# Optimization experiments

Measured on AMD Instinct MI355X. Metric: run time of the kernel, lower is better.

## Reference

```python
import jax, jax.numpy as jnp
import numpy as np

RMAX = 5.0   # max_radius
NB = 8       # bessel bases
NSH = 9      # (lmax+1)^2, lmax=2
S = 4        # message passing steps


def _rms(x):
    return x * jax.lax.rsqrt(jnp.mean(x * x, axis=-1, keepdims=True) + 1e-6)


def _mlp(x, w1, b1, w2, b2):
    # 2-layer MLP (base_mlp_depth=2) with silu activation + rms_norm output
    return _rms(jax.nn.silu(x @ w1 + b1) @ w2 + b2)


def _sh(u):
    # real spherical harmonics up to l=2, component normalization (e3nn style), u: [E,3] unit vectors
    x, y, z = u[:, 0], u[:, 1], u[:, 2]
    s3, s5, s15 = 3.0 ** 0.5, 5.0 ** 0.5, 15.0 ** 0.5
    return jnp.stack([
        jnp.ones_like(x),
        s3 * x, s3 * y, s3 * z,
        s15 * x * y, s15 * y * z, 0.5 * s5 * (3.0 * z * z - 1.0),
        s15 * x * z, 0.5 * s15 * (x * x - y * y)], axis=1)


def setup_inputs() -> dict:
    key = jax.random.key(0)
    ks = iter(jax.random.split(key, 64))
    N, E, D, H, L, BOND = 20000, 640000, 128, 256, 128, 16

    def w(shape, fan):
        return jax.random.normal(next(ks), shape, jnp.float32) / np.float32(np.sqrt(fan))

    return dict(
        pos=jax.random.normal(next(ks), (N, 3), jnp.float32),
        c_in=jnp.ones((1,), jnp.float32),
        atom_type_index=jax.random.randint(next(ks), (N,), 0, 20),
        atom_code_index=jax.random.randint(next(ks), (N,), 0, 10),
        residue_code_index=jax.random.randint(next(ks), (N,), 0, 25),
        residue_sequence_index=jnp.zeros((N,), jnp.int32),  # max_sequence_length=1
        senders=jax.random.randint(next(ks), (E,), 0, N),
        receivers=jax.random.randint(next(ks), (E,), 0, N),
        bond_mask=jax.random.randint(next(ks), (E,), 0, 2),
        emb_at=w((20, 32), 1.0), emb_ac=w((10, 32), 1.0),
        emb_rc=w((25, 32), 1.0), emb_ri=w((1, 32), 1.0),
        emb_bond=w((2, BOND), 1.0),
        nenc_w1=w((D, H), D), nenc_b1=jnp.zeros((H,), jnp.float32),
        nenc_w2=w((H, L), H), nenc_b2=jnp.zeros((L,), jnp.float32),
        eenc_w1=w((NB * NSH + BOND, H), NB * NSH + BOND), eenc_b1=jnp.zeros((H,), jnp.float32),
        eenc_w2=w((H, L), H), eenc_b2=jnp.zeros((L,), jnp.float32),
        msg_w1=w((S, 3 * L, H), 3 * L), msg_b1=jnp.zeros((S, H), jnp.float32),
        msg_w2=w((S, H, L), H), msg_b2=jnp.zeros((S, L), jnp.float32),
        gate_w=w((S, L, 1), L), gate_b=jnp.zeros((S, 1), jnp.float32),
        upd_w1=w((S, 2 * L, H), 2 * L), upd_b1=jnp.zeros((S, H), jnp.float32),
        upd_w2=w((S, H, L), H), upd_b2=jnp.zeros((S, L), jnp.float32),
        head_w1=w((L, H), L), head_b1=jnp.zeros((H,), jnp.float32),
        head_w2=w((H, 3), H), head_b2=jnp.zeros((3,), jnp.float32),
    )


def reference(pos, c_in, atom_type_index, atom_code_index, residue_code_index,
              residue_sequence_index, senders, receivers, bond_mask,
              emb_at, emb_ac, emb_rc, emb_ri, emb_bond,
              nenc_w1, nenc_b1, nenc_w2, nenc_b2,
              eenc_w1, eenc_b1, eenc_w2, eenc_b2,
              msg_w1, msg_b1, msg_w2, msg_b2, gate_w, gate_b,
              upd_w1, upd_b1, upd_w2, upd_b2,
              head_w1, head_b1, head_w2, head_b2):
    N = pos.shape[0]
    E = senders.shape[0]

    # --- update_features: embeddings + edge vectors ---
    node_emb = jnp.concatenate([
        emb_at[atom_type_index], emb_ac[atom_code_index],
        emb_rc[residue_code_index], emb_ri[residue_sequence_index]], axis=1)  # [N,128]
    bond_emb = emb_bond[bond_mask]                                            # [E,16]

    up = pos / c_in
    vec = up[senders] - up[receivers]                                         # [E,3]
    r = jnp.sqrt(jnp.sum(vec * vec, axis=-1) + 1e-12)                         # [E]
    u = vec / r[:, None]

    # Bessel RBF: sqrt(2/rmax) * sin(n*pi*r/rmax) / r
    n = jnp.arange(1, NB + 1, dtype=jnp.float32)
    rbf = jnp.sqrt(2.0 / RMAX) * jnp.sin(n[None, :] * jnp.pi * r[:, None] / RMAX) / r[:, None]
    # cosine distance cutoff envelope
    cut = 0.5 * (jnp.cos(jnp.pi * jnp.minimum(r, RMAX) / RMAX) + 1.0) * (r < RMAX)

    ylm = _sh(u)                                                              # [E,9]
    radial = (rbf[:, :, None] * ylm[:, None, :]).reshape(E, NB * NSH) * cut[:, None]

    # --- encoders ---
    h = _mlp(node_emb, nenc_w1, nenc_b1, nenc_w2, nenc_b2)                    # [N,L]
    e = _mlp(jnp.concatenate([radial, bond_emb], axis=1),
             eenc_w1, eenc_b1, eenc_w2, eenc_b2)                              # [E,L]

    # --- message passing: gather -> MLP -> sigmoid-gate * cutoff -> scatter ---
    for s in range(S):
        m = _mlp(jnp.concatenate([h[senders], h[receivers], e], axis=1),
                 msg_w1[s], msg_b1[s], msg_w2[s], msg_b2[s])                  # [E,L]
        g = jax.nn.sigmoid(m @ gate_w[s] + gate_b[s]) * cut[:, None]          # [E,1]
        agg = jax.ops.segment_sum(m * g, receivers, num_segments=N)           # [N,L]
        h = h + _mlp(jnp.concatenate([h, agg], axis=1),
                     upd_w1[s], upd_b1[s], upd_w2[s], upd_b2[s])
        e = e + m

    # --- head: predict per-node 3-vector ---
    return jax.nn.silu(h @ head_w1 + head_b1) @ head_w2 + head_b2             # [N,3]
```

## Files before the change

kernel.cpp:

```cpp
#include <hip/hip_runtime.h>
#include <hip/hip_bf16.h>
#include <math.h>


#define TILE   16
#define STRIDE 20

using short8 = __attribute__((ext_vector_type(8))) short;
using f32x4  = __attribute__((ext_vector_type(4))) float;

__device__ __forceinline__ float silu_f(float x) {
  return x / (1.0f + expf(-x));
}
__device__ __forceinline__ unsigned short f2b(float x) {
  union { float f; unsigned u; } v; v.f = x;
  unsigned r = v.u + 0x7fffu + ((v.u >> 16) & 1u);
  return (unsigned short)(r >> 16);
}
__device__ __forceinline__ float b2f(unsigned short h) {
  union { unsigned u; float f; } v; v.u = ((unsigned)h) << 16;
  return v.f;
}

__global__ __launch_bounds__(256) void pack_w_kernel(
    const float* __restrict__ src, unsigned short* __restrict__ dst,
    int Kreal, int KS, int NF)
{
  const int N = NF * 16;
  const int total = NF * KS * 512;
  for (int idx = blockIdx.x * 256 + threadIdx.x; idx < total; idx += gridDim.x * 256) {
    const int nf  = idx / (KS * 512);
    const int rem = idx - nf * (KS * 512);
    const int kk  = rem >> 9;
    const int p   = rem & 511;
    const int l   = p >> 3, j = p & 7;
    const int c   = nf * 16 + (l & 15);
    const int k   = kk * 32 + ((l >> 4) << 3) + j;
    dst[idx] = (k < Kreal) ? f2b(src[(size_t)k * N + c]) : (unsigned short)0;
  }
}

template<int KS1>
__device__ __forceinline__ void mfma_l1(const unsigned short* __restrict__ x1,
                                        const unsigned short* __restrict__ w1p,
                                        const float* __restrict__ b1,
                                        unsigned short* __restrict__ hsm, int tid)
{
  const int w  = tid >> 6;
  const int l  = tid & 63;
  const int lr = l & 15;
  const int lk = (l >> 4) << 3;
  const int RS = KS1 * 32;
  f32x4 acc[8];
  const f32x4 zz = {0.f, 0.f, 0.f, 0.f};
  #pragma unroll
  for (int i = 0; i < 8; ++i) acc[i] = zz;

  for (int kk = 0; kk < KS1; ++kk) {
    short8 af[2];
    #pragma unroll
    for (int mf = 0; mf < 2; ++mf) {
      const int r = mf * 16 + lr;
      const int k = kk * 32 + lk;
      af[mf] = *(const short8*)&x1[r * RS + ((((k >> 3) ^ (r & 7))) << 3)];
    }
    #pragma unroll
    for (int nf = 0; nf < 4; ++nf) {
      const int nfg = w * 4 + nf;
      const short8 bf = *(const short8*)&w1p[(size_t)(((nfg * KS1) + kk) * 64 + l) * 8];
      #pragma unroll
      for (int mf = 0; mf < 2; ++mf)
        acc[mf * 4 + nf] = __builtin_amdgcn_mfma_f32_16x16x32_bf16(af[mf], bf, acc[mf * 4 + nf], 0, 0, 0);
    }
  }
  #pragma unroll
  for (int nf = 0; nf < 4; ++nf) {
    const int c = (w * 4 + nf) * 16 + lr;
    const float bias = b1[c];
    #pragma unroll
    for (int mf = 0; mf < 2; ++mf) {
      #pragma unroll
      for (int q = 0; q < 4; ++q) {
        const int r = mf * 16 + ((l >> 4) << 2) + q;
        const float v = silu_f(acc[mf * 4 + nf][q] + bias);
        hsm[r * 256 + (((c >> 3) ^ (r & 7)) << 3) + (c & 7)] = f2b(v);
      }
    }
  }
}

__device__ __forceinline__ void mfma_l2(const unsigned short* __restrict__ hsm,
                                        const unsigned short* __restrict__ w2p,
                                        const float* __restrict__ b2,
                                        int tid, f32x4 acc2[4])
{
  const int w  = tid >> 6;
  const int l  = tid & 63;
  const int lr = l & 15;
  const int lk = (l >> 4) << 3;
  const f32x4 zz = {0.f, 0.f, 0.f, 0.f};
  #pragma unroll
  for (int i = 0; i < 4; ++i) acc2[i] = zz;

  for (int kk = 0; kk < 8; ++kk) {
    short8 af[2];
    #pragma unroll
    for (int mf = 0; mf < 2; ++mf) {
      const int r = mf * 16 + lr;
      const int k = kk * 32 + lk;
      af[mf] = *(const short8*)&hsm[r * 256 + (((k >> 3) ^ (r & 7)) << 3)];
    }
    #pragma unroll
    for (int nf2 = 0; nf2 < 2; ++nf2) {
      const int nfg = w * 2 + nf2;
      const short8 bf = *(const short8*)&w2p[(size_t)(((nfg * 8) + kk) * 64 + l) * 8];
      #pragma unroll
      for (int mf = 0; mf < 2; ++mf)
        acc2[mf * 2 + nf2] = __builtin_amdgcn_mfma_f32_16x16x32_bf16(af[mf], bf, acc2[mf * 2 + nf2], 0, 0, 0);
    }
  }
  #pragma unroll
  for (int nf2 = 0; nf2 < 2; ++nf2) {
    const float bias = b2[(w * 2 + nf2) * 16 + lr];
    #pragma unroll
    for (int mf = 0; mf < 2; ++mf) {
      #pragma unroll
      for (int q = 0; q < 4; ++q) acc2[mf * 2 + nf2][q] += bias;
    }
  }
}

__device__ __forceinline__ void rms_reduce(const f32x4 acc2[4], float* rsum,
                                           int tid, float mval[2][2][4])
{
  const int l = tid & 63;
  #pragma unroll
  for (int mf = 0; mf < 2; ++mf) {
    #pragma unroll
    for (int q = 0; q < 4; ++q) {
      float s = acc2[mf * 2][q] * acc2[mf * 2][q]
              + acc2[mf * 2 + 1][q] * acc2[mf * 2 + 1][q];
      s += __shfl_xor(s, 1); s += __shfl_xor(s, 2);
      s += __shfl_xor(s, 4); s += __shfl_xor(s, 8);
      if ((l & 15) == 0)
        atomicAdd(&rsum[mf * 16 + ((l >> 4) << 2) + q], s);
    }
  }
  __syncthreads();
  #pragma unroll
  for (int mf = 0; mf < 2; ++mf) {
    #pragma unroll
    for (int q = 0; q < 4; ++q) {
      const int r = mf * 16 + ((l >> 4) << 2) + q;
      const float inv = rsqrtf(rsum[r] * (1.0f / 128.0f) + 1e-6f);
      #pragma unroll
      for (int nf2 = 0; nf2 < 2; ++nf2)
        mval[mf][nf2][q] = acc2[mf * 2 + nf2][q] * inv;
    }
  }
}

__global__ __launch_bounds__(256, 3) void edge_enc_mfma(
    const float* __restrict__ pos, const float* __restrict__ c_in,
    const int* __restrict__ snd, const int* __restrict__ rcv,
    const int* __restrict__ bnd, const float* __restrict__ embb,
    const unsigned short* __restrict__ w1p, const float* __restrict__ b1,
    const unsigned short* __restrict__ w2p, const float* __restrict__ b2,
    unsigned short* __restrict__ e_g, float* __restrict__ cutb, int E)
{
  __shared__ __align__(16) unsigned short x1[32 * 128];
  __shared__ __align__(16) unsigned short hsm[32 * 256];
  __shared__ float grbf[32][8];
  __shared__ float gylm[32][9];
  __shared__ float gcut[32];
  __shared__ int   gbond[32];
  __shared__ float rsum[32];
  const int tid = threadIdx.x;
  const int e0  = blockIdx.x * 32;

  if (tid < 32) {
    rsum[tid] = 0.f;
    const int ed = min(e0 + tid, E - 1);
    const int sa = snd[ed], ra = rcv[ed];
    const float ci = c_in[0];
    const float vx = (pos[sa * 3 + 0] - pos[ra * 3 + 0]) / ci;
    const float vy = (pos[sa * 3 + 1] - pos[ra * 3 + 1]) / ci;
    const float vz = (pos[sa * 3 + 2] - pos[ra * 3 + 2]) / ci;
    const float r  = sqrtf(vx * vx + vy * vy + vz * vz + 1e-12f);
    const float ir = 1.0f / r;
    const float ux = vx * ir, uy = vy * ir, uz = vz * ir;
    const float PI = 3.14159265358979323846f;
    const float pr = PI * r * 0.2f;
    const float c0 = 0.632455532033675866f;
    #pragma unroll
    for (int n = 0; n < 8; ++n)
      grbf[tid][n] = c0 * sinf((float)(n + 1) * pr) * ir;
    const float cv = 0.5f * (cosf(PI * fminf(r, 5.0f) * 0.2f) + 1.0f)
                   * (r < 5.0f ? 1.0f : 0.0f);
    gcut[tid] = cv;
    if (e0 + tid < E) cutb[e0 + tid] = cv;
    const float s3  = 1.7320508075688772f;
    const float s5  = 2.2360679774997896f;
    const float s15 = 3.8729833462074170f;
    gylm[tid][0] = 1.0f;
    gylm[tid][1] = s3 * ux; gylm[tid][2] = s3 * uy; gylm[tid][3] = s3 * uz;
    gylm[tid][4] = s15 * ux * uy; gylm[tid][5] = s15 * uy * uz;
    gylm[tid][6] = 0.5f * s5 * (3.0f * uz * uz - 1.0f);
    gylm[tid][7] = s15 * ux * uz;
    gylm[tid][8] = 0.5f * s15 * (ux * ux - uy * uy);
    gbond[tid] = bnd[ed];
  }
  __syncthreads();
  for (int i = tid; i < 32 * 16; i += 256) {
    const int r = i >> 4, g = i & 15;
    union { short8 v; unsigned short u[8]; } t;
    #pragma unroll
    for (int j = 0; j < 8; ++j) {
      const int k = g * 8 + j;
      float v;
      if (k < 72) { const int n = k / 9, mm = k - 9 * n; v = grbf[r][n] * gylm[r][mm] * gcut[r]; }
      else if (k < 88) v = embb[gbond[r] * 16 + (k - 72)];
      else v = 0.f;
      t.u[j] = f2b(v);
    }
    *(short8*)&x1[r * 128 + ((g ^ (r & 7)) << 3)] = t.v;
  }
  __syncthreads();
  mfma_l1<4>(x1, w1p, b1, hsm, tid);
  __syncthreads();
  f32x4 acc2[4];
  mfma_l2(hsm, w2p, b2, tid, acc2);
  float mval[2][2][4];
  rms_reduce(acc2, rsum, tid, mval);
  const int l = tid & 63, w = tid >> 6, lr = l & 15;
  #pragma unroll
  for (int mf = 0; mf < 2; ++mf) {
    #pragma unroll
    for (int q = 0; q < 4; ++q) {
      const int r = mf * 16 + ((l >> 4) << 2) + q;
      const int ed = e0 + r;
      if (ed < E) {
        #pragma unroll
        for (int nf2 = 0; nf2 < 2; ++nf2) {
          const int c2 = (w * 2 + nf2) * 16 + lr;
          e_g[(size_t)ed * 128 + c2] = f2b(mval[mf][nf2][q]);
        }
      }
    }
  }
}

__global__ __launch_bounds__(256, 3) void msg_mfma(
    const float* __restrict__ h, unsigned short* __restrict__ e_g,
    float* __restrict__ agg, const float* __restrict__ cutb,
    const int* __restrict__ snd, const int* __restrict__ rcv,
    const unsigned short* __restrict__ w1p, const float* __restrict__ b1,
    const unsigned short* __restrict__ w2p, const float* __restrict__ b2,
    const float* __restrict__ gw, const float* __restrict__ gb, int E)
{
  __shared__ __align__(16) unsigned short x1[32 * 384];
  __shared__ __align__(16) unsigned short hsm[32 * 256];
  __shared__ int   snd_s[32], rcv_s[32];
  __shared__ float cut_s[32];
  __shared__ float rsum[32], gsum[32];
  const int tid = threadIdx.x;
  const int e0  = blockIdx.x * 32;

  if (tid < 32) {
    rsum[tid] = 0.f; gsum[tid] = 0.f;
    const int ed = min(e0 + tid, E - 1);
    snd_s[tid] = snd[ed]; rcv_s[tid] = rcv[ed]; cut_s[tid] = cutb[ed];
  }
  __syncthreads();
  for (int i = tid; i < 32 * 48; i += 256) {
    const int r = i / 48, g = i - r * 48;
    union { short8 v; unsigned short u[8]; } t;
    if (g < 32) {
      const int node = (g < 16) ? snd_s[r] : rcv_s[r];
      const int k0 = (g & 15) * 8;
      const float4 f0 = *(const float4*)&h[(size_t)node * 128 + k0];
      const float4 f1 = *(const float4*)&h[(size_t)node * 128 + k0 + 4];
      t.u[0] = f2b(f0.x); t.u[1] = f2b(f0.y); t.u[2] = f2b(f0.z); t.u[3] = f2b(f0.w);
      t.u[4] = f2b(f1.x); t.u[5] = f2b(f1.y); t.u[6] = f2b(f1.z); t.u[7] = f2b(f1.w);
    } else {
      const int ed = min(e0 + r, E - 1);
      t.v = *(const short8*)&e_g[(size_t)ed * 128 + (g - 32) * 8];
    }
    *(short8*)&x1[r * 384 + ((g ^ (r & 7)) << 3)] = t.v;
  }
  __syncthreads();
  mfma_l1<12>(x1, w1p, b1, hsm, tid);
  __syncthreads();
  f32x4 acc2[4];
  mfma_l2(hsm, w2p, b2, tid, acc2);
  float mval[2][2][4];
  rms_reduce(acc2, rsum, tid, mval);

  const int l = tid & 63, w = tid >> 6, lr = l & 15;
  const float gw0 = gw[(w * 2 + 0) * 16 + lr];
  const float gw1 = gw[(w * 2 + 1) * 16 + lr];
  #pragma unroll
  for (int mf = 0; mf < 2; ++mf) {
    #pragma unroll
    for (int q = 0; q < 4; ++q) {
      float p = mval[mf][0][q] * gw0 + mval[mf][1][q] * gw1;
      p += __shfl_xor(p, 1); p += __shfl_xor(p, 2);
      p += __shfl_xor(p, 4); p += __shfl_xor(p, 8);
      if ((l & 15) == 0)
        atomicAdd(&gsum[mf * 16 + ((l >> 4) << 2) + q], p);
    }
  }
  __syncthreads();
  const float gbv = gb[0];
  #pragma unroll
  for (int mf = 0; mf < 2; ++mf) {
    #pragma unroll
    for (int q = 0; q < 4; ++q) {
      const int r = mf * 16 + ((l >> 4) << 2) + q;
      const int ed = e0 + r;
      if (ed < E) {
        const float gr = cut_s[r] / (1.0f + expf(-(gsum[r] + gbv)));
        const int rv = rcv_s[r];
        #pragma unroll
        for (int nf2 = 0; nf2 < 2; ++nf2) {
          const int c2 = (w * 2 + nf2) * 16 + lr;
          const float m = mval[mf][nf2][q];
          const int k = 256 + c2;
          const float eo = b2f(x1[r * 384 + (((k >> 3) ^ (r & 7)) << 3) + (k & 7)]);
          e_g[(size_t)ed * 128 + c2] = f2b(eo + m);
          atomicAdd(&agg[(size_t)rv * 128 + c2], m * gr);
        }
      }
    }
  }
}

__global__ __launch_bounds__(256, 3) void upd_mfma(
    float* __restrict__ h, const float* __restrict__ agg,
    const unsigned short* __restrict__ w1p, const float* __restrict__ b1,
    const unsigned short* __restrict__ w2p, const float* __restrict__ b2,
    int N)
{
  __shared__ __align__(16) unsigned short x1[32 * 256];
  __shared__ __align__(16) unsigned short hsm[32 * 256];
  __shared__ float rsum[32];
  const int tid = threadIdx.x;
  const int n0  = blockIdx.x * 32;
  if (tid < 32) rsum[tid] = 0.f;
  __syncthreads();
  for (int i = tid; i < 32 * 32; i += 256) {
    const int r = i >> 5, g = i & 31;
    const int n = min(n0 + r, N - 1);
    const float* src = (g < 16) ? &h[(size_t)n * 128 + g * 8]
                                : &agg[(size_t)n * 128 + (g - 16) * 8];
    const float4 f0 = *(const float4*)src;
    const float4 f1 = *(const float4*)(src + 4);
    union { short8 v; unsigned short u[8]; } t;
    t.u[0] = f2b(f0.x); t.u[1] = f2b(f0.y); t.u[2] = f2b(f0.z); t.u[3] = f2b(f0.w);
    t.u[4] = f2b(f1.x); t.u[5] = f2b(f1.y); t.u[6] = f2b(f1.z); t.u[7] = f2b(f1.w);
    *(short8*)&x1[r * 256 + ((g ^ (r & 7)) << 3)] = t.v;
  }
  __syncthreads();
  mfma_l1<8>(x1, w1p, b1, hsm, tid);
  __syncthreads();
  f32x4 acc2[4];
  mfma_l2(hsm, w2p, b2, tid, acc2);
  float mval[2][2][4];
  rms_reduce(acc2, rsum, tid, mval);
  const int l = tid & 63, w = tid >> 6, lr = l & 15;
  #pragma unroll
  for (int mf = 0; mf < 2; ++mf) {
    #pragma unroll
    for (int q = 0; q < 4; ++q) {
      const int r = mf * 16 + ((l >> 4) << 2) + q;
      const int n = n0 + r;
      if (n < N) {
        #pragma unroll
        for (int nf2 = 0; nf2 < 2; ++nf2) {
          const int c2 = (w * 2 + nf2) * 16 + lr;
          h[(size_t)n * 128 + c2] += mval[mf][nf2][q];
        }
      }
    }
  }
}


__device__ __forceinline__ float loadE(const float* p)          { return *p; }
__device__ __forceinline__ float loadE(const __hip_bfloat16* p) { return __bfloat162float(*p); }
__device__ __forceinline__ void  storeE(float* p, float v)          { *p = v; }
__device__ __forceinline__ void  storeE(__hip_bfloat16* p, float v) { *p = __float2bfloat16(v); }

template<int K1>
__device__ __forceinline__ void layer1_silu(const float* __restrict__ xs,
                                            const float* __restrict__ w1,
                                            const float* __restrict__ b1,
                                            float* __restrict__ hs, int tid)
{
  const int jh = tid & 127;
  const int tp = tid >> 7;
  const int tbase = 8 * tp;
  float a[8] = {0,0,0,0,0,0,0,0};
  float b[8] = {0,0,0,0,0,0,0,0};
  const float* wp = w1 + jh;
  for (int k = 0; k < K1; ++k) {
    const float4 x0 = *(const float4*)&xs[k*STRIDE + tbase];
    const float4 x1 = *(const float4*)&xs[k*STRIDE + tbase + 4];
    const float wa = wp[k*256];
    const float wb = wp[k*256 + 128];
    a[0] = fmaf(x0.x, wa, a[0]); a[1] = fmaf(x0.y, wa, a[1]);
    a[2] = fmaf(x0.z, wa, a[2]); a[3] = fmaf(x0.w, wa, a[3]);
    a[4] = fmaf(x1.x, wa, a[4]); a[5] = fmaf(x1.y, wa, a[5]);
    a[6] = fmaf(x1.z, wa, a[6]); a[7] = fmaf(x1.w, wa, a[7]);
    b[0] = fmaf(x0.x, wb, b[0]); b[1] = fmaf(x0.y, wb, b[1]);
    b[2] = fmaf(x0.z, wb, b[2]); b[3] = fmaf(x0.w, wb, b[3]);
    b[4] = fmaf(x1.x, wb, b[4]); b[5] = fmaf(x1.y, wb, b[5]);
    b[6] = fmaf(x1.z, wb, b[6]); b[7] = fmaf(x1.w, wb, b[7]);
  }
  const float ba = b1[jh];
  const float bb = b1[jh + 128];
  float4 oa0, oa1, ob0, ob1;
  oa0.x = silu_f(a[0] + ba); oa0.y = silu_f(a[1] + ba);
  oa0.z = silu_f(a[2] + ba); oa0.w = silu_f(a[3] + ba);
  oa1.x = silu_f(a[4] + ba); oa1.y = silu_f(a[5] + ba);
  oa1.z = silu_f(a[6] + ba); oa1.w = silu_f(a[7] + ba);
  ob0.x = silu_f(b[0] + bb); ob0.y = silu_f(b[1] + bb);
  ob0.z = silu_f(b[2] + bb); ob0.w = silu_f(b[3] + bb);
  ob1.x = silu_f(b[4] + bb); ob1.y = silu_f(b[5] + bb);
  ob1.z = silu_f(b[6] + bb); ob1.w = silu_f(b[7] + bb);
  *(float4*)&hs[jh*STRIDE + tbase]           = oa0;
  *(float4*)&hs[jh*STRIDE + tbase + 4]       = oa1;
  *(float4*)&hs[(jh+128)*STRIDE + tbase]     = ob0;
  *(float4*)&hs[(jh+128)*STRIDE + tbase + 4] = ob1;
}

__device__ __forceinline__ void layer2_bias(const float* __restrict__ hs,
                                            const float* __restrict__ w2,
                                            const float* __restrict__ b2,
                                            int tid, float cA[4], float cB[4])
{
  const int dh = tid & 63;
  const int tq = tid >> 6;
  const int tbase = 4 * tq;
  cA[0]=cA[1]=cA[2]=cA[3]=0.0f;
  cB[0]=cB[1]=cB[2]=cB[3]=0.0f;
  const float* wp = w2 + dh;
  for (int k = 0; k < 256; ++k) {
    const float4 hv = *(const float4*)&hs[k*STRIDE + tbase];
    const float wa = wp[k*128];
    const float wb = wp[k*128 + 64];
    cA[0] = fmaf(hv.x, wa, cA[0]); cA[1] = fmaf(hv.y, wa, cA[1]);
    cA[2] = fmaf(hv.z, wa, cA[2]); cA[3] = fmaf(hv.w, wa, cA[3]);
    cB[0] = fmaf(hv.x, wb, cB[0]); cB[1] = fmaf(hv.y, wb, cB[1]);
    cB[2] = fmaf(hv.z, wb, cB[2]); cB[3] = fmaf(hv.w, wb, cB[3]);
  }
  const float b2a = b2[dh];
  const float b2b = b2[dh + 64];
  #pragma unroll
  for (int tt = 0; tt < 4; ++tt) { cA[tt] += b2a; cB[tt] += b2b; }
}

__device__ __forceinline__ void rms4(float cA[4], float cB[4])
{
  float s[4];
  #pragma unroll
  for (int tt = 0; tt < 4; ++tt) s[tt] = cA[tt]*cA[tt] + cB[tt]*cB[tt];
  #pragma unroll
  for (int off = 32; off; off >>= 1) {
    #pragma unroll
    for (int tt = 0; tt < 4; ++tt) s[tt] += __shfl_xor(s[tt], off);
  }
  #pragma unroll
  for (int tt = 0; tt < 4; ++tt) {
    const float inv = rsqrtf(s[tt] * (1.0f/128.0f) + 1e-6f);
    cA[tt] *= inv; cB[tt] *= inv;
  }
}

__global__ __launch_bounds__(256) void zero_kernel(float4* __restrict__ p, int n4)
{
  const int i = blockIdx.x * 256 + threadIdx.x;
  if (i < n4) p[i] = make_float4(0.f, 0.f, 0.f, 0.f);
}

__global__ __launch_bounds__(256) void node_enc_kernel(
    const int* __restrict__ ati, const int* __restrict__ aci,
    const int* __restrict__ rci, const int* __restrict__ rsi,
    const float* __restrict__ emb_at, const float* __restrict__ emb_ac,
    const float* __restrict__ emb_rc, const float* __restrict__ emb_ri,
    const float* __restrict__ w1, const float* __restrict__ b1,
    const float* __restrict__ w2, const float* __restrict__ b2,
    float* __restrict__ h, int N)
{
  __shared__ __align__(16) float xs[128*STRIDE];
  __shared__ __align__(16) float hs[256*STRIDE];
  __shared__ int idx_s[4][TILE];
  const int tid = threadIdx.x;
  const int n0 = blockIdx.x * TILE;
  if (tid < TILE) {
    const int n = min(n0 + tid, N - 1);
    idx_s[0][tid] = ati[n]; idx_s[1][tid] = aci[n];
    idx_s[2][tid] = rci[n]; idx_s[3][tid] = rsi[n];
  }
  __syncthreads();
  for (int i = tid; i < TILE*128; i += 256) {
    const int t = i >> 7, k = i & 127;
    const int seg = k >> 5, kk = k & 31;
    const float* tab = (seg == 0) ? emb_at : (seg == 1) ? emb_ac
                     : (seg == 2) ? emb_rc : emb_ri;
    xs[k*STRIDE + t] = tab[idx_s[seg][t]*32 + kk];
  }
  __syncthreads();
  layer1_silu<128>(xs, w1, b1, hs, tid);
  __syncthreads();
  float cA[4], cB[4];
  layer2_bias(hs, w2, b2, tid, cA, cB);
  rms4(cA, cB);
  const int dh = tid & 63, tq = tid >> 6;
  #pragma unroll
  for (int tt = 0; tt < 4; ++tt) {
    const int n = n0 + 4*tq + tt;
    if (n < N) {
      h[(size_t)n*128 + dh]      = cA[tt];
      h[(size_t)n*128 + dh + 64] = cB[tt];
    }
  }
}

template<typename ET>
__global__ __launch_bounds__(256) void edge_enc_kernel(
    const float* __restrict__ pos, const float* __restrict__ c_in,
    const int* __restrict__ snd, const int* __restrict__ rcv,
    const int* __restrict__ bnd, const float* __restrict__ emb_bond,
    const float* __restrict__ w1, const float* __restrict__ b1,
    const float* __restrict__ w2, const float* __restrict__ b2,
    ET* __restrict__ e, float* __restrict__ cutb, int E)
{
  __shared__ __align__(16) float xs[88*STRIDE];
  __shared__ __align__(16) float hs[256*STRIDE];
  __shared__ float grbf[TILE][8];
  __shared__ float gylm[TILE][9];
  __shared__ float gcut[TILE];
  __shared__ int   gbond[TILE];
  const int tid = threadIdx.x;
  const int e0 = blockIdx.x * TILE;
  if (tid < TILE) {
    const int ed = min(e0 + tid, E - 1);
    const int sa = snd[ed], ra = rcv[ed];
    const float ci = c_in[0];
    const float vx = (pos[sa*3+0] - pos[ra*3+0]) / ci;
    const float vy = (pos[sa*3+1] - pos[ra*3+1]) / ci;
    const float vz = (pos[sa*3+2] - pos[ra*3+2]) / ci;
    const float r  = sqrtf(vx*vx + vy*vy + vz*vz + 1e-12f);
    const float ir = 1.0f / r;
    const float ux = vx*ir, uy = vy*ir, uz = vz*ir;
    const float PI = 3.14159265358979323846f;
    const float pr = PI * r * 0.2f;
    const float c0 = 0.632455532033675866f;
    #pragma unroll
    for (int n = 0; n < 8; ++n)
      grbf[tid][n] = c0 * sinf((float)(n + 1) * pr) * ir;
    const float cv = 0.5f * (cosf(PI * fminf(r, 5.0f) * 0.2f) + 1.0f)
                   * (r < 5.0f ? 1.0f : 0.0f);
    gcut[tid] = cv;
    cutb[ed] = cv;
    const float s3  = 1.7320508075688772f;
    const float s5  = 2.2360679774997896f;
    const float s15 = 3.8729833462074170f;
    gylm[tid][0] = 1.0f;
    gylm[tid][1] = s3*ux; gylm[tid][2] = s3*uy; gylm[tid][3] = s3*uz;
    gylm[tid][4] = s15*ux*uy; gylm[tid][5] = s15*uy*uz;
    gylm[tid][6] = 0.5f*s5*(3.0f*uz*uz - 1.0f);
    gylm[tid][7] = s15*ux*uz;
    gylm[tid][8] = 0.5f*s15*(ux*ux - uy*uy);
    gbond[tid] = bnd[ed];
  }
  __syncthreads();
  for (int i = tid; i < TILE*88; i += 256) {
    const int t = i & 15, k = i >> 4;
    float v;
    if (k < 72) {
      const int n = k / 9, m = k - 9*n;
      v = grbf[t][n] * gylm[t][m] * gcut[t];
    } else {
      v = emb_bond[gbond[t]*16 + (k - 72)];
    }
    xs[k*STRIDE + t] = v;
  }
  __syncthreads();
  layer1_silu<88>(xs, w1, b1, hs, tid);
  __syncthreads();
  float cA[4], cB[4];
  layer2_bias(hs, w2, b2, tid, cA, cB);
  rms4(cA, cB);
  const int dh = tid & 63, tq = tid >> 6;
  #pragma unroll
  for (int tt = 0; tt < 4; ++tt) {
    const int ed = e0 + 4*tq + tt;
    if (ed < E) {
      storeE(&e[(size_t)ed*128 + dh],      cA[tt]);
      storeE(&e[(size_t)ed*128 + dh + 64], cB[tt]);
    }
  }
}

template<typename ET>
__global__ __launch_bounds__(256) void msg_kernel(
    const float* __restrict__ h, ET* __restrict__ e,
    float* __restrict__ agg, const float* __restrict__ cutb,
    const int* __restrict__ snd, const int* __restrict__ rcv,
    const float* __restrict__ w1, const float* __restrict__ b1,
    const float* __restrict__ w2, const float* __restrict__ b2,
    const float* __restrict__ gw, const float* __restrict__ gb,
    int E)
{
  __shared__ __align__(16) float xs[384*STRIDE];
  __shared__ __align__(16) float hs[256*STRIDE];
  __shared__ int   snd_s[TILE], rcv_s[TILE];
  __shared__ float cut_s[TILE];
  const int tid = threadIdx.x;
  const int e0 = blockIdx.x * TILE;
  if (tid < TILE) {
    const int ed = min(e0 + tid, E - 1);
    snd_s[tid] = snd[ed]; rcv_s[tid] = rcv[ed]; cut_s[tid] = cutb[ed];
  }
  __syncthreads();
  for (int i = tid; i < TILE*384; i += 256) {
    const int t = i / 384, k = i - t*384;
    float v;
    if (k < 128)      v = h[(size_t)snd_s[t]*128 + k];
    else if (k < 256) v = h[(size_t)rcv_s[t]*128 + (k - 128)];
    else {
      const int ed = min(e0 + t, E - 1);
      v = loadE(&e[(size_t)ed*128 + (k - 256)]);
    }
    xs[k*STRIDE + t] = v;
  }
  __syncthreads();
  layer1_silu<384>(xs, w1, b1, hs, tid);
  __syncthreads();
  float cA[4], cB[4];
  layer2_bias(hs, w2, b2, tid, cA, cB);
  rms4(cA, cB);
  const int dh = tid & 63, tq = tid >> 6;
  const float gwa = gw[dh], gwb = gw[dh + 64];
  const float gbv = gb[0];
  float gv[4];
  #pragma unroll
  for (int tt = 0; tt < 4; ++tt) gv[tt] = cA[tt]*gwa + cB[tt]*gwb;
  #pragma unroll
  for (int off = 32; off; off >>= 1) {
    #pragma unroll
    for (int tt = 0; tt < 4; ++tt) gv[tt] += __shfl_xor(gv[tt], off);
  }
  #pragma unroll
  for (int tt = 0; tt < 4; ++tt) {
    const int t = 4*tq + tt;
    const int ed = e0 + t;
    if (ed < E) {
      const float g = cut_s[t] / (1.0f + expf(-(gv[tt] + gbv)));
      const float eoA = xs[(256 + dh)*STRIDE + t];
      const float eoB = xs[(256 + dh + 64)*STRIDE + t];
      storeE(&e[(size_t)ed*128 + dh],      eoA + cA[tt]);
      storeE(&e[(size_t)ed*128 + dh + 64], eoB + cB[tt]);
      const int rv = rcv_s[t];
      atomicAdd(&agg[(size_t)rv*128 + dh],      cA[tt]*g);
      atomicAdd(&agg[(size_t)rv*128 + dh + 64], cB[tt]*g);
    }
  }
}

__global__ __launch_bounds__(256) void upd_kernel(
    float* __restrict__ h, const float* __restrict__ agg,
    const float* __restrict__ w1, const float* __restrict__ b1,
    const float* __restrict__ w2, const float* __restrict__ b2,
    int N)
{
  __shared__ __align__(16) float xs[256*STRIDE];
  __shared__ __align__(16) float hs[256*STRIDE];
  const int tid = threadIdx.x;
  const int n0 = blockIdx.x * TILE;
  for (int i = tid; i < TILE*256; i += 256) {
    const int t = i >> 8, k = i & 255;
    const int n = min(n0 + t, N - 1);
    const float v = (k < 128) ? h[(size_t)n*128 + k]
                              : agg[(size_t)n*128 + (k - 128)];
    xs[k*STRIDE + t] = v;
  }
  __syncthreads();
  layer1_silu<256>(xs, w1, b1, hs, tid);
  __syncthreads();
  float cA[4], cB[4];
  layer2_bias(hs, w2, b2, tid, cA, cB);
  rms4(cA, cB);
  const int dh = tid & 63, tq = tid >> 6;
  #pragma unroll
  for (int tt = 0; tt < 4; ++tt) {
    const int t = 4*tq + tt;
    const int n = n0 + t;
    if (n < N) {
      h[(size_t)n*128 + dh]      = xs[dh*STRIDE + t] + cA[tt];
      h[(size_t)n*128 + dh + 64] = xs[(dh + 64)*STRIDE + t] + cB[tt];
    }
  }
}

__global__ __launch_bounds__(256) void head_kernel(
    const float* __restrict__ h,
    const float* __restrict__ w1, const float* __restrict__ b1,
    const float* __restrict__ w2, const float* __restrict__ b2,
    float* __restrict__ out, int N)
{
  __shared__ __align__(16) float xs[128*STRIDE];
  __shared__ __align__(16) float hs[256*STRIDE];
  const int tid = threadIdx.x;
  const int n0 = blockIdx.x * TILE;
  for (int i = tid; i < TILE*128; i += 256) {
    const int t = i >> 7, k = i & 127;
    const int n = min(n0 + t, N - 1);
    xs[k*STRIDE + t] = h[(size_t)n*128 + k];
  }
  __syncthreads();
  layer1_silu<128>(xs, w1, b1, hs, tid);
  __syncthreads();
  if (tid < 48) {
    const int t = tid / 3, o = tid - 3*(tid/3);
    float acc = b2[o];
    for (int k = 0; k < 256; ++k)
      acc = fmaf(hs[k*STRIDE + t], w2[k*3 + o], acc);
    const int n = n0 + t;
    if (n < N) out[(size_t)n*3 + o] = acc;
  }
}

extern "C" void kernel_launch(void* const* d_in, const int* in_sizes, int n_in,
                              void* d_out, int out_size, void* d_ws, size_t ws_size,
                              hipStream_t stream)
{
  const float* pos      = (const float*)d_in[0];
  const float* c_in     = (const float*)d_in[1];
  const int*   ati      = (const int*)d_in[2];
  const int*   aci      = (const int*)d_in[3];
  const int*   rci      = (const int*)d_in[4];
  const int*   rsi      = (const int*)d_in[5];
  const int*   snd      = (const int*)d_in[6];
  const int*   rcv      = (const int*)d_in[7];
  const int*   bnd      = (const int*)d_in[8];
  const float* emb_at   = (const float*)d_in[9];
  const float* emb_ac   = (const float*)d_in[10];
  const float* emb_rc   = (const float*)d_in[11];
  const float* emb_ri   = (const float*)d_in[12];
  const float* emb_bond = (const float*)d_in[13];
  const float* nenc_w1  = (const float*)d_in[14];
  const float* nenc_b1  = (const float*)d_in[15];
  const float* nenc_w2  = (const float*)d_in[16];
  const float* nenc_b2  = (const float*)d_in[17];
  const float* eenc_w1  = (const float*)d_in[18];
  const float* eenc_b1  = (const float*)d_in[19];
  const float* eenc_w2  = (const float*)d_in[20];
  const float* eenc_b2  = (const float*)d_in[21];
  const float* msg_w1   = (const float*)d_in[22];
  const float* msg_b1   = (const float*)d_in[23];
  const float* msg_w2   = (const float*)d_in[24];
  const float* msg_b2   = (const float*)d_in[25];
  const float* gate_w   = (const float*)d_in[26];
  const float* gate_b   = (const float*)d_in[27];
  const float* upd_w1   = (const float*)d_in[28];
  const float* upd_b1   = (const float*)d_in[29];
  const float* upd_w2   = (const float*)d_in[30];
  const float* upd_b2   = (const float*)d_in[31];
  const float* head_w1  = (const float*)d_in[32];
  const float* head_b1  = (const float*)d_in[33];
  const float* head_w2  = (const float*)d_in[34];
  const float* head_b2  = (const float*)d_in[35];

  const int N = in_sizes[0] / 3;
  const int E = in_sizes[6];

  char* ws = (char*)d_ws;
  float* hbuf   = (float*)ws;                   ws += (size_t)N * 128 * sizeof(float);
  float* aggbuf = (float*)ws;                   ws += (size_t)N * 128 * sizeof(float);
  float* cutbuf = (float*)ws;                   ws += (size_t)E * sizeof(float);
  unsigned short* packs = (unsigned short*)ws;
  const size_t eenc_w1p_o = 0;
  const size_t eenc_w2p_o = eenc_w1p_o + 16*4*512;
  const size_t msg_w1p_o  = eenc_w2p_o + 8*8*512;
  const size_t msg_w2p_o  = msg_w1p_o + 4*(size_t)(16*12*512);
  const size_t upd_w1p_o  = msg_w2p_o + 4*(size_t)(8*8*512);
  const size_t upd_w2p_o  = upd_w1p_o + 4*(size_t)(16*8*512);
  const size_t packs_end  = upd_w2p_o + 4*(size_t)(8*8*512);
  ws += packs_end * sizeof(unsigned short);
  unsigned short* ebuf_mfma = (unsigned short*)ws;
  const size_t need_mfma = (size_t)(ws - (char*)d_ws) + (size_t)E * 128 * sizeof(unsigned short);

  const int nb_n16 = (N + TILE - 1) / TILE;
  const int n4     = N * 128 / 4;

  if (ws_size >= need_mfma) {
    const int nb_e32 = (E + 31) / 32;
    const int nb_n32 = (N + 31) / 32;

    pack_w_kernel<<<96, 256, 0, stream>>>(eenc_w1, packs + eenc_w1p_o, 88, 4, 16);
    pack_w_kernel<<<96, 256, 0, stream>>>(eenc_w2, packs + eenc_w2p_o, 256, 8, 8);
    for (int s = 0; s < 4; ++s) {
      pack_w_kernel<<<96, 256, 0, stream>>>(msg_w1 + (size_t)s*384*256,
          packs + msg_w1p_o + (size_t)s*16*12*512, 384, 12, 16);
      pack_w_kernel<<<96, 256, 0, stream>>>(msg_w2 + (size_t)s*256*128,
          packs + msg_w2p_o + (size_t)s*8*8*512, 256, 8, 8);
      pack_w_kernel<<<96, 256, 0, stream>>>(upd_w1 + (size_t)s*256*256,
          packs + upd_w1p_o + (size_t)s*16*8*512, 256, 8, 16);
      pack_w_kernel<<<96, 256, 0, stream>>>(upd_w2 + (size_t)s*256*128,
          packs + upd_w2p_o + (size_t)s*8*8*512, 256, 8, 8);
    }

    node_enc_kernel<<<nb_n16, 256, 0, stream>>>(
        ati, aci, rci, rsi, emb_at, emb_ac, emb_rc, emb_ri,
        nenc_w1, nenc_b1, nenc_w2, nenc_b2, hbuf, N);

    edge_enc_mfma<<<nb_e32, 256, 0, stream>>>(
        pos, c_in, snd, rcv, bnd, emb_bond,
        packs + eenc_w1p_o, eenc_b1, packs + eenc_w2p_o, eenc_b2,
        ebuf_mfma, cutbuf, E);

    for (int s = 0; s < 4; ++s) {
      zero_kernel<<<(n4 + 255) / 256, 256, 0, stream>>>((float4*)aggbuf, n4);
      msg_mfma<<<nb_e32, 256, 0, stream>>>(
          hbuf, ebuf_mfma, aggbuf, cutbuf, snd, rcv,
          packs + msg_w1p_o + (size_t)s*16*12*512, msg_b1 + (size_t)s*256,
          packs + msg_w2p_o + (size_t)s*8*8*512,   msg_b2 + (size_t)s*128,
          gate_w + (size_t)s*128, gate_b + s, E);
      upd_mfma<<<nb_n32, 256, 0, stream>>>(
          hbuf, aggbuf,
          packs + upd_w1p_o + (size_t)s*16*8*512, upd_b1 + (size_t)s*256,
          packs + upd_w2p_o + (size_t)s*8*8*512,  upd_b2 + (size_t)s*128, N);
    }

    head_kernel<<<nb_n16, 256, 0, stream>>>(
        hbuf, head_w1, head_b1, head_w2, head_b2, (float*)d_out, N);
  } else {
    __hip_bfloat16* ebuf = (__hip_bfloat16*)((char*)d_ws
        + (size_t)N*128*4 + (size_t)N*128*4 + (size_t)E*4);
    const int nb_e16 = (E + TILE - 1) / TILE;

    node_enc_kernel<<<nb_n16, 256, 0, stream>>>(
        ati, aci, rci, rsi, emb_at, emb_ac, emb_rc, emb_ri,
        nenc_w1, nenc_b1, nenc_w2, nenc_b2, hbuf, N);

    edge_enc_kernel<__hip_bfloat16><<<nb_e16, 256, 0, stream>>>(
        pos, c_in, snd, rcv, bnd, emb_bond,
        eenc_w1, eenc_b1, eenc_w2, eenc_b2, ebuf, cutbuf, E);

    for (int s = 0; s < 4; ++s) {
      zero_kernel<<<(n4 + 255) / 256, 256, 0, stream>>>((float4*)aggbuf, n4);
      msg_kernel<__hip_bfloat16><<<nb_e16, 256, 0, stream>>>(
          hbuf, ebuf, aggbuf, cutbuf, snd, rcv,
          msg_w1 + (size_t)s * 384 * 256, msg_b1 + (size_t)s * 256,
          msg_w2 + (size_t)s * 256 * 128, msg_b2 + (size_t)s * 128,
          gate_w + (size_t)s * 128, gate_b + s, E);
      upd_kernel<<<nb_n16, 256, 0, stream>>>(
          hbuf, aggbuf,
          upd_w1 + (size_t)s * 256 * 256, upd_b1 + (size_t)s * 256,
          upd_w2 + (size_t)s * 256 * 128, upd_b2 + (size_t)s * 128, N);
    }

    head_kernel<<<nb_n16, 256, 0, stream>>>(
        hbuf, head_w1, head_b1, head_w2, head_b2, (float*)d_out, N);
  }
}
```

Baseline: 2.731 ms.

## Alias LDS buffers, keep a bf16 shadow of node features, raise occupancy

The input-staging and hidden-activation LDS buffers in the edge-encoder, message and update kernels now share one allocation. An extra barrier separates the first-layer MFMA from the silu store, which cuts LDS use enough to request 5 blocks per CU instead of 3. A bf16 copy of node features is kept next to the fp32 one, so the message kernel gathers half the bytes per sender and receiver row and skips the conversion. Both copies are written in the node encoder and the update kernel. The message kernel now re-reads the old edge state from global memory instead of LDS, and silu and the gate use fast __expf. Costs are an extra barrier, an extra global read per edge element, and the 5-block bound may force register spills.

New measurement: 2.463 ms. -9.8%, faster.

```diff
diff --git a/kernel.cpp b/kernel.cpp
--- a/kernel.cpp
+++ b/kernel.cpp
@@ -10,7 +10,7 @@
 using f32x4  = __attribute__((ext_vector_type(4))) float;
 
 __device__ __forceinline__ float silu_f(float x) {
-  return x / (1.0f + expf(-x));
+  return x / (1.0f + __expf(-x));
 }
 __device__ __forceinline__ unsigned short f2b(float x) {
   union { float f; unsigned u; } v; v.f = x;
@@ -41,17 +41,15 @@
 }
 
 template<int KS1>
-__device__ __forceinline__ void mfma_l1(const unsigned short* __restrict__ x1,
-                                        const unsigned short* __restrict__ w1p,
-                                        const float* __restrict__ b1,
-                                        unsigned short* __restrict__ hsm, int tid)
+__device__ __forceinline__ void mfma_l1_compute(const unsigned short* __restrict__ x1,
+                                                const unsigned short* __restrict__ w1p,
+                                                int tid, f32x4 acc[8])
 {
   const int w  = tid >> 6;
   const int l  = tid & 63;
   const int lr = l & 15;
   const int lk = (l >> 4) << 3;
   const int RS = KS1 * 32;
-  f32x4 acc[8];
   const f32x4 zz = {0.f, 0.f, 0.f, 0.f};
   #pragma unroll
   for (int i = 0; i < 8; ++i) acc[i] = zz;
@@ -73,6 +71,14 @@
         acc[mf * 4 + nf] = __builtin_amdgcn_mfma_f32_16x16x32_bf16(af[mf], bf, acc[mf * 4 + nf], 0, 0, 0);
     }
   }
+}
+
+__device__ __forceinline__ void l1_store_silu(const f32x4 acc[8],
+                                              const float* __restrict__ b1,
+                                              unsigned short* __restrict__ hsm,
+                                              int tid)
+{
+  const int w = tid >> 6, l = tid & 63, lr = l & 15;
   #pragma unroll
   for (int nf = 0; nf < 4; ++nf) {
     const int c = (w * 4 + nf) * 16 + lr;
@@ -160,7 +166,7 @@
   }
 }
 
-__global__ __launch_bounds__(256, 3) void edge_enc_mfma(
+__global__ __launch_bounds__(256, 5) void edge_enc_mfma(
     const float* __restrict__ pos, const float* __restrict__ c_in,
     const int* __restrict__ snd, const int* __restrict__ rcv,
     const int* __restrict__ bnd, const float* __restrict__ embb,
@@ -168,8 +174,9 @@
     const unsigned short* __restrict__ w2p, const float* __restrict__ b2,
     unsigned short* __restrict__ e_g, float* __restrict__ cutb, int E)
 {
-  __shared__ __align__(16) unsigned short x1[32 * 128];
-  __shared__ __align__(16) unsigned short hsm[32 * 256];
+  __shared__ __align__(16) unsigned short smem[32 * 256];
+  unsigned short* x1  = smem;
+  unsigned short* hsm = smem;
   __shared__ float grbf[32][8];
   __shared__ float gylm[32][9];
   __shared__ float gcut[32];
@@ -226,7 +233,10 @@
     *(short8*)&x1[r * 128 + ((g ^ (r & 7)) << 3)] = t.v;
   }
   __syncthreads();
-  mfma_l1<4>(x1, w1p, b1, hsm, tid);
+  f32x4 acc1[8];
+  mfma_l1_compute<4>(x1, w1p, tid, acc1);
+  __syncthreads();
+  l1_store_silu(acc1, b1, hsm, tid);
   __syncthreads();
   f32x4 acc2[4];
   mfma_l2(hsm, w2p, b2, tid, acc2);
@@ -250,16 +260,17 @@
   }
 }
 
-__global__ __launch_bounds__(256, 3) void msg_mfma(
-    const float* __restrict__ h, unsigned short* __restrict__ e_g,
+__global__ __launch_bounds__(256, 5) void msg_mfma(
+    const unsigned short* __restrict__ hb, unsigned short* __restrict__ e_g,
     float* __restrict__ agg, const float* __restrict__ cutb,
     const int* __restrict__ snd, const int* __restrict__ rcv,
     const unsigned short* __restrict__ w1p, const float* __restrict__ b1,
     const unsigned short* __restrict__ w2p, const float* __restrict__ b2,
     const float* __restrict__ gw, const float* __restrict__ gb, int E)
 {
-  __shared__ __align__(16) unsigned short x1[32 * 384];
-  __shared__ __align__(16) unsigned short hsm[32 * 256];
+  __shared__ __align__(16) unsigned short smem[32 * 384];
+  unsigned short* x1  = smem;
+  unsigned short* hsm = smem;
   __shared__ int   snd_s[32], rcv_s[32];
   __shared__ float cut_s[32];
   __shared__ float rsum[32], gsum[32];
@@ -274,22 +285,21 @@
   __syncthreads();
   for (int i = tid; i < 32 * 48; i += 256) {
     const int r = i / 48, g = i - r * 48;
-    union { short8 v; unsigned short u[8]; } t;
+    short8 t;
     if (g < 32) {
       const int node = (g < 16) ? snd_s[r] : rcv_s[r];
-      const int k0 = (g & 15) * 8;
-      const float4 f0 = *(const float4*)&h[(size_t)node * 128 + k0];
-      const float4 f1 = *(const float4*)&h[(size_t)node * 128 + k0 + 4];
-      t.u[0] = f2b(f0.x); t.u[1] = f2b(f0.y); t.u[2] = f2b(f0.z); t.u[3] = f2b(f0.w);
-      t.u[4] = f2b(f1.x); t.u[5] = f2b(f1.y); t.u[6] = f2b(f1.z); t.u[7] = f2b(f1.w);
+      t = *(const short8*)&hb[(size_t)node * 128 + (g & 15) * 8];
     } else {
       const int ed = min(e0 + r, E - 1);
-      t.v = *(const short8*)&e_g[(size_t)ed * 128 + (g - 32) * 8];
-    }
-    *(short8*)&x1[r * 384 + ((g ^ (r & 7)) << 3)] = t.v;
-  }
-  __syncthreads();
-  mfma_l1<12>(x1, w1p, b1, hsm, tid);
+      t = *(const short8*)&e_g[(size_t)ed * 128 + (g - 32) * 8];
+    }
+    *(short8*)&x1[r * 384 + ((g ^ (r & 7)) << 3)] = t;
+  }
+  __syncthreads();
+  f32x4 acc1[8];
+  mfma_l1_compute<12>(x1, w1p, tid, acc1);
+  __syncthreads();
+  l1_store_silu(acc1, b1, hsm, tid);
   __syncthreads();
   f32x4 acc2[4];
   mfma_l2(hsm, w2p, b2, tid, acc2);
@@ -319,14 +329,13 @@
       const int r = mf * 16 + ((l >> 4) << 2) + q;
       const int ed = e0 + r;
       if (ed < E) {
-        const float gr = cut_s[r] / (1.0f + expf(-(gsum[r] + gbv)));
+        const float gr = cut_s[r] / (1.0f + __expf(-(gsum[r] + gbv)));
         const int rv = rcv_s[r];
         #pragma unroll
         for (int nf2 = 0; nf2 < 2; ++nf2) {
           const int c2 = (w * 2 + nf2) * 16 + lr;
           const float m = mval[mf][nf2][q];
-          const int k = 256 + c2;
-          const float eo = b2f(x1[r * 384 + (((k >> 3) ^ (r & 7)) << 3) + (k & 7)]);
+          const float eo = b2f(e_g[(size_t)ed * 128 + c2]);
           e_g[(size_t)ed * 128 + c2] = f2b(eo + m);
           atomicAdd(&agg[(size_t)rv * 128 + c2], m * gr);
         }
@@ -335,14 +344,16 @@
   }
 }
 
-__global__ __launch_bounds__(256, 3) void upd_mfma(
-    float* __restrict__ h, const float* __restrict__ agg,
+__global__ __launch_bounds__(256, 5) void upd_mfma(
+    float* __restrict__ h, unsigned short* __restrict__ hb,
+    const float* __restrict__ agg,
     const unsigned short* __restrict__ w1p, const float* __restrict__ b1,
     const unsigned short* __restrict__ w2p, const float* __restrict__ b2,
     int N)
 {
-  __shared__ __align__(16) unsigned short x1[32 * 256];
-  __shared__ __align__(16) unsigned short hsm[32 * 256];
+  __shared__ __align__(16) unsigned short smem[32 * 256];
+  unsigned short* x1  = smem;
+  unsigned short* hsm = smem;
   __shared__ float rsum[32];
   const int tid = threadIdx.x;
   const int n0  = blockIdx.x * 32;
@@ -351,17 +362,24 @@
   for (int i = tid; i < 32 * 32; i += 256) {
     const int r = i >> 5, g = i & 31;
     const int n = min(n0 + r, N - 1);
-    const float* src = (g < 16) ? &h[(size_t)n * 128 + g * 8]
-                                : &agg[(size_t)n * 128 + (g - 16) * 8];
-    const float4 f0 = *(const float4*)src;
-    const float4 f1 = *(const float4*)(src + 4);
-    union { short8 v; unsigned short u[8]; } t;
-    t.u[0] = f2b(f0.x); t.u[1] = f2b(f0.y); t.u[2] = f2b(f0.z); t.u[3] = f2b(f0.w);
-    t.u[4] = f2b(f1.x); t.u[5] = f2b(f1.y); t.u[6] = f2b(f1.z); t.u[7] = f2b(f1.w);
-    *(short8*)&x1[r * 256 + ((g ^ (r & 7)) << 3)] = t.v;
-  }
-  __syncthreads();
-  mfma_l1<8>(x1, w1p, b1, hsm, tid);
+    short8 t;
+    if (g < 16) {
+      t = *(const short8*)&hb[(size_t)n * 128 + g * 8];
+    } else {
+      const float4 f0 = *(const float4*)&agg[(size_t)n * 128 + (g - 16) * 8];
+      const float4 f1 = *(const float4*)&agg[(size_t)n * 128 + (g - 16) * 8 + 4];
+      union { short8 v; unsigned short u[8]; } tt;
+      tt.u[0] = f2b(f0.x); tt.u[1] = f2b(f0.y); tt.u[2] = f2b(f0.z); tt.u[3] = f2b(f0.w);
+      tt.u[4] = f2b(f1.x); tt.u[5] = f2b(f1.y); tt.u[6] = f2b(f1.z); tt.u[7] = f2b(f1.w);
+      t = tt.v;
+    }
+    *(short8*)&x1[r * 256 + ((g ^ (r & 7)) << 3)] = t;
+  }
+  __syncthreads();
+  f32x4 acc1[8];
+  mfma_l1_compute<8>(x1, w1p, tid, acc1);
+  __syncthreads();
+  l1_store_silu(acc1, b1, hsm, tid);
   __syncthreads();
   f32x4 acc2[4];
   mfma_l2(hsm, w2p, b2, tid, acc2);
@@ -378,7 +396,9 @@
         #pragma unroll
         for (int nf2 = 0; nf2 < 2; ++nf2) {
           const int c2 = (w * 2 + nf2) * 16 + lr;
-          h[(size_t)n * 128 + c2] += mval[mf][nf2][q];
+          const float nh = h[(size_t)n * 128 + c2] + mval[mf][nf2][q];
+          h[(size_t)n * 128 + c2]  = nh;
+          hb[(size_t)n * 128 + c2] = f2b(nh);
         }
       }
     }
@@ -490,7 +510,7 @@
     const float* __restrict__ emb_rc, const float* __restrict__ emb_ri,
     const float* __restrict__ w1, const float* __restrict__ b1,
     const float* __restrict__ w2, const float* __restrict__ b2,
-    float* __restrict__ h, int N)
+    float* __restrict__ h, unsigned short* __restrict__ hb, int N)
 {
   __shared__ __align__(16) float xs[128*STRIDE];
   __shared__ __align__(16) float hs[256*STRIDE];
@@ -523,6 +543,10 @@
     if (n < N) {
       h[(size_t)n*128 + dh]      = cA[tt];
       h[(size_t)n*128 + dh + 64] = cB[tt];
+      if (hb) {
+        hb[(size_t)n*128 + dh]      = f2b(cA[tt]);
+        hb[(size_t)n*128 + dh + 64] = f2b(cB[tt]);
+      }
     }
   }
 }
@@ -658,7 +682,7 @@
     const int t = 4*tq + tt;
     const int ed = e0 + t;
     if (ed < E) {
-      const float g = cut_s[t] / (1.0f + expf(-(gv[tt] + gbv)));
+      const float g = cut_s[t] / (1.0f + __expf(-(gv[tt] + gbv)));
       const float eoA = xs[(256 + dh)*STRIDE + t];
       const float eoB = xs[(256 + dh + 64)*STRIDE + t];
       storeE(&e[(size_t)ed*128 + dh],      eoA + cA[tt]);
@@ -778,9 +802,10 @@
   const int E = in_sizes[6];
 
   char* ws = (char*)d_ws;
-  float* hbuf   = (float*)ws;                   ws += (size_t)N * 128 * sizeof(float);
-  float* aggbuf = (float*)ws;                   ws += (size_t)N * 128 * sizeof(float);
-  float* cutbuf = (float*)ws;                   ws += (size_t)E * sizeof(float);
+  float* hbuf           = (float*)ws;           ws += (size_t)N * 128 * sizeof(float);
+  unsigned short* hbb   = (unsigned short*)ws;  ws += (size_t)N * 128 * sizeof(unsigned short);
+  float* aggbuf         = (float*)ws;           ws += (size_t)N * 128 * sizeof(float);
+  float* cutbuf         = (float*)ws;           ws += (size_t)E * sizeof(float);
   unsigned short* packs = (unsigned short*)ws;
   const size_t eenc_w1p_o = 0;
   const size_t eenc_w2p_o = eenc_w1p_o + 16*4*512;
@@ -815,7 +840,7 @@
 
     node_enc_kernel<<<nb_n16, 256, 0, stream>>>(
         ati, aci, rci, rsi, emb_at, emb_ac, emb_rc, emb_ri,
-        nenc_w1, nenc_b1, nenc_w2, nenc_b2, hbuf, N);
+        nenc_w1, nenc_b1, nenc_w2, nenc_b2, hbuf, hbb, N);
 
     edge_enc_mfma<<<nb_e32, 256, 0, stream>>>(
         pos, c_in, snd, rcv, bnd, emb_bond,
@@ -825,12 +850,12 @@
     for (int s = 0; s < 4; ++s) {
       zero_kernel<<<(n4 + 255) / 256, 256, 0, stream>>>((float4*)aggbuf, n4);
       msg_mfma<<<nb_e32, 256, 0, stream>>>(
-          hbuf, ebuf_mfma, aggbuf, cutbuf, snd, rcv,
+          hbb, ebuf_mfma, aggbuf, cutbuf, snd, rcv,
           packs + msg_w1p_o + (size_t)s*16*12*512, msg_b1 + (size_t)s*256,
           packs + msg_w2p_o + (size_t)s*8*8*512,   msg_b2 + (size_t)s*128,
           gate_w + (size_t)s*128, gate_b + s, E);
       upd_mfma<<<nb_n32, 256, 0, stream>>>(
-          hbuf, aggbuf,
+          hbuf, hbb, aggbuf,
           packs + upd_w1p_o + (size_t)s*16*8*512, upd_b1 + (size_t)s*256,
           packs + upd_w2p_o + (size_t)s*8*8*512,  upd_b2 + (size_t)s*128, N);
     }
@@ -838,32 +863,35 @@
     head_kernel<<<nb_n16, 256, 0, stream>>>(
         hbuf, head_w1, head_b1, head_w2, head_b2, (float*)d_out, N);
   } else {
-    __hip_bfloat16* ebuf = (__hip_bfloat16*)((char*)d_ws
-        + (size_t)N*128*4 + (size_t)N*128*4 + (size_t)E*4);
+    char* ws2 = (char*)d_ws;
+    float* hbuf2   = (float*)ws2;   ws2 += (size_t)N * 128 * sizeof(float);
+    float* aggbuf2 = (float*)ws2;   ws2 += (size_t)N * 128 * sizeof(float);
+    float* cutbuf2 = (float*)ws2;   ws2 += (size_t)E * sizeof(float);
+    __hip_bfloat16* ebuf = (__hip_bfloat16*)ws2;
     const int nb_e16 = (E + TILE - 1) / TILE;
 
     node_enc_kernel<<<nb_n16, 256, 0, stream>>>(
         ati, aci, rci, rsi, emb_at, emb_ac, emb_rc, emb_ri,
-        nenc_w1, nenc_b1, nenc_w2, nenc_b2, hbuf, N);
+        nenc_w1, nenc_b1, nenc_w2, nenc_b2, hbuf2, (unsigned short*)nullptr, N);
 
     edge_enc_kernel<__hip_bfloat16><<<nb_e16, 256, 0, stream>>>(
         pos, c_in, snd, rcv, bnd, emb_bond,
-        eenc_w1, eenc_b1, eenc_w2, eenc_b2, ebuf, cutbuf, E);
+        eenc_w1, eenc_b1, eenc_w2, eenc_b2, ebuf, cutbuf2, E);
 
     for (int s = 0; s < 4; ++s) {
-      zero_kernel<<<(n4 + 255) / 256, 256, 0, stream>>>((float4*)aggbuf, n4);
+      zero_kernel<<<(n4 + 255) / 256, 256, 0, stream>>>((float4*)aggbuf2, n4);
       msg_kernel<__hip_bfloat16><<<nb_e16, 256, 0, stream>>>(
-          hbuf, ebuf, aggbuf, cutbuf, snd, rcv,
+          hbuf2, ebuf, aggbuf2, cutbuf2, snd, rcv,
           msg_w1 + (size_t)s * 384 * 256, msg_b1 + (size_t)s * 256,
           msg_w2 + (size_t)s * 256 * 128, msg_b2 + (size_t)s * 128,
           gate_w + (size_t)s * 128, gate_b + s, E);
       upd_kernel<<<nb_n16, 256, 0, stream>>>(
-          hbuf, aggbuf,
+          hbuf2, aggbuf2,
           upd_w1 + (size_t)s * 256 * 256, upd_b1 + (size_t)s * 256,
           upd_w2 + (size_t)s * 256 * 128, upd_b2 + (size_t)s * 128, N);
     }
 
     head_kernel<<<nb_n16, 256, 0, stream>>>(
-        hbuf, head_w1, head_b1, head_w2, head_b2, (float*)d_out, N);
-  }
-}
+        hbuf2, head_w1, head_b1, head_w2, head_b2, (float*)d_out, N);
+  }
+}
```
